# Optimization experiments

Measured on AMD Instinct MI355X. Metric: run time of the kernel, lower is better.

## Reference

```python
import jax, jax.numpy as jnp
import numpy as np

N = 50000   # nodes
E = 800000  # edges
F = 64      # input features
H = 64      # hidden (nhid)
C = 10      # classes
G = 500     # graphs in batch


def setup_inputs() -> dict:
    key = jax.random.key(0)
    ks = jax.random.split(key, 12)
    s = lambda fan: np.float32(1.0 / np.sqrt(fan))
    return {
        "x": jax.random.normal(ks[0], (N, F), jnp.float32),
        "edge_index": jax.random.randint(ks[1], (2, E), 0, N, dtype=jnp.int64),
        "batch": jnp.sort(jax.random.randint(ks[2], (N,), 0, G, dtype=jnp.int64)),
        "W1": jax.random.normal(ks[3], (F, H), jnp.float32) * s(F),
        "b1": jnp.zeros((H,), jnp.float32),
        "W2": jax.random.normal(ks[4], (H, H), jnp.float32) * s(H),
        "b2": jnp.zeros((H,), jnp.float32),
        "W3": jax.random.normal(ks[5], (H, H), jnp.float32) * s(H),
        "b3": jnp.zeros((H,), jnp.float32),
        "lin1_W": jax.random.normal(ks[6], (H, H), jnp.float32) * s(H),
        "lin1_b": jnp.zeros((H,), jnp.float32),
        "lin2_W": jax.random.normal(ks[7], (H, C), jnp.float32) * s(H),
        "lin2_b": jnp.zeros((C,), jnp.float32),
    }


def reference(x, edge_index, batch, W1, b1, W2, b2, W3, b3, lin1_W, lin1_b, lin2_W, lin2_b):
    n = x.shape[0]
    loops = jnp.arange(n, dtype=edge_index.dtype)
    src = jnp.concatenate([edge_index[0], loops])  # message sources (x_j)
    dst = jnp.concatenate([edge_index[1], loops])  # aggregation targets
    # symmetric GCN normalization on A + I
    deg = jax.ops.segment_sum(jnp.ones(src.shape, x.dtype), dst, num_segments=n)
    dis = jax.lax.rsqrt(deg)  # deg >= 1 thanks to self-loops
    norm = (dis[src] * dis[dst])[:, None]  # [E+N, 1]

    def gcn_relu(h, W, b):
        h = h @ W                                   # [N, H]
        agg = jax.ops.segment_sum(h[src] * norm, dst, num_segments=n)
        return jax.nn.relu(agg + b)

    h = gcn_relu(x, W1, b1)
    h = gcn_relu(h, W2, b2)
    h = gcn_relu(h, W3, b3)

    # global mean pool per graph
    sums = jax.ops.segment_sum(h, batch, num_segments=G)
    counts = jax.ops.segment_sum(jnp.ones((n,), h.dtype), batch, num_segments=G)
    pooled = sums / jnp.maximum(counts, 1.0)[:, None]  # [G, H]

    h = jax.nn.relu(pooled @ lin1_W + lin1_b)
    # dropout is identity in eval mode
    logits = h @ lin2_W + lin2_b
    return jax.nn.log_softmax(logits, axis=-1)
```

## Files before the change

### kernel.cpp

```cpp
#include <hip/hip_runtime.h>

#define NN 50000
#define NE 800000
#define HD 64
#define NC 10
#define NG 500
#define CAP 64
#define NBLK 196
#define NPART 8
#define PSZ 6250
#define FILLB 2048
#define NPW 8

__device__ __forceinline__ float bf16_to_f32(unsigned short h) {
    union { unsigned int u; float f; } v;
    v.u = ((unsigned int)h) << 16;
    return v.f;
}
__device__ __forceinline__ unsigned short f32_to_bf16(float f) {
    union { float f; unsigned int u; } v;
    v.f = f;
    unsigned int r = v.u + 0x7FFFu + ((v.u >> 16) & 1u);
    return (unsigned short)(r >> 16);
}

__global__ void init_k(int* __restrict__ rowcnt) {
    int i = blockIdx.x * 256 + threadIdx.x;
    if (i < NN) rowcnt[i] = 0;
}

__global__ __launch_bounds__(256) void fill3_k(
    const int* __restrict__ src, const int* __restrict__ dst,
    int* __restrict__ rowcnt, unsigned short* __restrict__ col16) {
    int part = blockIdx.x & (NPART - 1);
    int blk = blockIdx.x >> 3;
    int dlo = part * PSZ, dhi = dlo + PSZ;
    int stride = (FILLB / NPART) * 256;
    for (int e = blk * 256 + threadIdx.x; e < NE; e += stride) {
        int d = dst[e];
        if (d >= dlo && d < dhi) {
            int p = atomicAdd(&rowcnt[d], 1);
            if (p < CAP) col16[(size_t)d * CAP + p] = (unsigned short)src[e];
        }
    }
}

__global__ __launch_bounds__(256) void gemm64_k(const float* __restrict__ in,
                                                const float* __restrict__ W,
                                                const int* __restrict__ rowcnt,
                                                unsigned short* __restrict__ out16) {
    __shared__ float Ws[64 * 64];
    int t = threadIdx.x;
    for (int k = t; k < 64 * 64; k += 256) Ws[k] = W[k];
    __syncthreads();
    int lane = t & 63;
    int rgrp = t >> 6;
    int row0 = blockIdx.x * 16 + rgrp * 4;
#pragma unroll
    for (int rr = 0; rr < 4; ++rr) {
        int row = row0 + rr;
        const float4* h4 = (const float4*)(in + (size_t)row * HD);
        float acc = 0.f;
#pragma unroll
        for (int k4 = 0; k4 < 16; ++k4) {
            float4 h = h4[k4];
            acc += h.x * Ws[(k4 * 4 + 0) * 64 + lane];
            acc += h.y * Ws[(k4 * 4 + 1) * 64 + lane];
            acc += h.z * Ws[(k4 * 4 + 2) * 64 + lane];
            acc += h.w * Ws[(k4 * 4 + 3) * 64 + lane];
        }
        float di = rsqrtf((float)(rowcnt[row] + 1));
        out16[(size_t)row * HD + lane] = f32_to_bf16(acc * di);
    }
}

__global__ __launch_bounds__(256) void aggemm_k(
    const unsigned short* __restrict__ tin, const int* __restrict__ rowcnt,
    const unsigned short* __restrict__ col16, const float* __restrict__ bias,
    const float* __restrict__ Wn, unsigned short* __restrict__ tout) {
    __shared__ float Ws[64 * 64];
    __shared__ float rbuf[4][64];
    int t = threadIdx.x;
    for (int k = t; k < 64 * 64; k += 256) Ws[k] = Wn[k];
    __syncthreads();
    int w = t >> 6, lane = t & 63;
    float bv = bias[lane];
    int base = (blockIdx.x * 4 + w) * NPW;
    for (int n = 0; n < NPW; ++n) {
        int wid = base + n;
        bool valid = wid < NN;
        float r = 0.f, di = 1.f;
        if (valid) {
            int colv = col16[(size_t)wid * CAP + lane];
            int c0 = rowcnt[wid];
            di = rsqrtf((float)(c0 + 1));
            int cnt = c0 > CAP ? CAP : c0;
            float acc[8];
#pragma unroll
            for (int j = 0; j < 8; ++j) acc[j] = 0.f;
            acc[0] = bf16_to_f32(tin[(size_t)wid * HD + lane]);
            int e = 0;
            for (; e + 7 < cnt; e += 8) {
#pragma unroll
                for (int j = 0; j < 8; ++j) {
                    int s = __shfl(colv, e + j);
                    acc[j] += bf16_to_f32(tin[(size_t)s * HD + lane]);
                }
            }
            for (; e < cnt; ++e) {
                int s = __shfl(colv, e);
                acc[0] += bf16_to_f32(tin[(size_t)s * HD + lane]);
            }
            float s01 = (acc[0] + acc[1]) + (acc[2] + acc[3]);
            float s23 = (acc[4] + acc[5]) + (acc[6] + acc[7]);
            r = fmaxf((s01 + s23) * di + bv, 0.f);
        }
        rbuf[w][lane] = r;
        __builtin_amdgcn_wave_barrier();
        float acc2 = 0.f;
        const float4* rb4 = (const float4*)rbuf[w];
#pragma unroll
        for (int k4 = 0; k4 < 16; ++k4) {
            float4 rv = rb4[k4];
            acc2 += rv.x * Ws[(k4 * 4 + 0) * 64 + lane];
            acc2 += rv.y * Ws[(k4 * 4 + 1) * 64 + lane];
            acc2 += rv.z * Ws[(k4 * 4 + 2) * 64 + lane];
            acc2 += rv.w * Ws[(k4 * 4 + 3) * 64 + lane];
        }
        if (valid) tout[(size_t)wid * HD + lane] = f32_to_bf16(acc2 * di);
        __builtin_amdgcn_wave_barrier();
    }
}

__global__ __launch_bounds__(256) void agg_k(
    const unsigned short* __restrict__ tin, const int* __restrict__ rowcnt,
    const unsigned short* __restrict__ col16, const float* __restrict__ bias,
    float* __restrict__ out) {
    int wid = blockIdx.x * 4 + (threadIdx.x >> 6);
    int lane = threadIdx.x & 63;
    if (wid >= NN) return;
    int colv = col16[(size_t)wid * CAP + lane];
    int c0 = rowcnt[wid];
    float di = rsqrtf((float)(c0 + 1));
    int cnt = c0 > CAP ? CAP : c0;
    float acc[8];
#pragma unroll
    for (int j = 0; j < 8; ++j) acc[j] = 0.f;
    acc[0] = bf16_to_f32(tin[(size_t)wid * HD + lane]);
    int e = 0;
    for (; e + 7 < cnt; e += 8) {
#pragma unroll
        for (int j = 0; j < 8; ++j) {
            int s = __shfl(colv, e + j);
            acc[j] += bf16_to_f32(tin[(size_t)s * HD + lane]);
        }
    }
    for (; e < cnt; ++e) {
        int s = __shfl(colv, e);
        acc[0] += bf16_to_f32(tin[(size_t)s * HD + lane]);
    }
    float s01 = (acc[0] + acc[1]) + (acc[2] + acc[3]);
    float s23 = (acc[4] + acc[5]) + (acc[6] + acc[7]);
    out[(size_t)wid * HD + lane] = fmaxf((s01 + s23) * di + bias[lane], 0.f);
}

__global__ __launch_bounds__(256) void poolhead_k(
    const float* __restrict__ h, const int* __restrict__ batch,
    const float* __restrict__ l1W, const float* __restrict__ l1b,
    const float* __restrict__ l2W, const float* __restrict__ l2b,
    float* __restrict__ out) {
    __shared__ float part[4][64];
    __shared__ float p[64];
    __shared__ float hsm[64];
    __shared__ float lg[NC];
    __shared__ int ss[2];
    int g = blockIdx.x;
    int t = threadIdx.x, lane = t & 63, w = t >> 6;
    if (t < 2) {
        int target = g + t;
        int lo = 0, hi = NN;
        while (lo < hi) {
            int mid = (lo + hi) >> 1;
            if (batch[mid] < target) lo = mid + 1; else hi = mid;
        }
        ss[t] = lo;
    }
    __syncthreads();
    int s0 = ss[0], s1 = ss[1];
    float acc = 0.f;
    for (int i = s0 + w; i < s1; i += 4) acc += h[(size_t)i * HD + lane];
    part[w][lane] = acc;
    __syncthreads();
    if (t < 64) {
        float s = part[0][t] + part[1][t] + part[2][t] + part[3][t];
        float c = (float)(s1 - s0);
        p[t] = s / fmaxf(c, 1.0f);
    }
    __syncthreads();
    if (t < 64) {
        float a = l1b[t];
#pragma unroll
        for (int k = 0; k < 64; ++k) a += p[k] * l1W[k * 64 + t];
        hsm[t] = fmaxf(a, 0.f);
    }
    __syncthreads();
    if (t < NC) {
        float a = l2b[t];
#pragma unroll
        for (int k = 0; k < 64; ++k) a += hsm[k] * l2W[k * NC + t];
        lg[t] = a;
    }
    __syncthreads();
    if (t < NC) {
        float m = -1e30f;
#pragma unroll
        for (int k = 0; k < NC; ++k) m = fmaxf(m, lg[k]);
        float s = 0.f;
#pragma unroll
        for (int k = 0; k < NC; ++k) s += expf(lg[k] - m);
        out[(size_t)g * NC + t] = lg[t] - m - logf(s);
    }
}

extern "C" void kernel_launch(void* const* d_in, const int* in_sizes, int n_in,
                              void* d_out, int out_size, void* d_ws, size_t ws_size,
                              hipStream_t stream) {
    const float* x = (const float*)d_in[0];
    const int* ei = (const int*)d_in[1];
    const int* src = ei;
    const int* dst = ei + NE;
    const int* batch = (const int*)d_in[2];
    const float* W1 = (const float*)d_in[3];
    const float* b1 = (const float*)d_in[4];
    const float* W2 = (const float*)d_in[5];
    const float* b2 = (const float*)d_in[6];
    const float* W3 = (const float*)d_in[7];
    const float* b3 = (const float*)d_in[8];
    const float* l1W = (const float*)d_in[9];
    const float* l1b = (const float*)d_in[10];
    const float* l2W = (const float*)d_in[11];
    const float* l2b = (const float*)d_in[12];
    float* out = (float*)d_out;

    char* p = (char*)d_ws;
    auto alloc = [&](size_t bytes) {
        char* r = p;
        p += (bytes + 255) & ~(size_t)255;
        return r;
    };
    int* rowcnt = (int*)alloc(NN * 4);
    unsigned short* col16 = (unsigned short*)alloc((size_t)NN * CAP * 2);
    unsigned short* tmpA = (unsigned short*)alloc((size_t)NN * HD * 2);
    unsigned short* tmpB = (unsigned short*)alloc((size_t)NN * HD * 2);
    float* hcur = (float*)alloc((size_t)NN * HD * 4);

    const int AGB = (NN + 4 * NPW - 1) / (4 * NPW);

    init_k<<<NBLK, 256, 0, stream>>>(rowcnt);
    fill3_k<<<FILLB, 256, 0, stream>>>(src, dst, rowcnt, col16);

    gemm64_k<<<3125, 256, 0, stream>>>(x, W1, rowcnt, tmpA);
    aggemm_k<<<AGB, 256, 0, stream>>>(tmpA, rowcnt, col16, b1, W2, tmpB);
    aggemm_k<<<AGB, 256, 0, stream>>>(tmpB, rowcnt, col16, b2, W3, tmpA);
    agg_k<<<(NN + 3) / 4, 256, 0, stream>>>(tmpA, rowcnt, col16, b3, hcur);

    poolhead_k<<<NG, 256, 0, stream>>>(hcur, batch, l1W, l1b, l2W, l2b, out);
}
```

Baseline: 279.0 us.

## Use bf16 MFMA with split-weight precision for the 64x64 GCN transforms

Replaces the scalar FMA dense transforms (first-layer GEMM and the fused aggregate-then-GEMM kernels) with 16x16x32 bf16 MFMA instructions. The weights are split into high and low bf16 parts so the result stays close to fp32 on the weight side, while activations are rounded to bf16. The fused kernel now aggregates 64 rows per block into shared memory and then runs one block-wide MFMA tile, replacing per-row LDS dot products. This adds extra MFMA work for the split weights, keeps the weights in registers per wave, and lowers activation precision for the first layer's input.

```diff
diff --git a/kernel.cpp b/kernel.cpp
--- a/kernel.cpp
+++ b/kernel.cpp
@@ -10,7 +10,10 @@
 #define NPART 8
 #define PSZ 6250
 #define FILLB 2048
-#define NPW 8
+#define MBLK 782
+
+typedef float f32x4 __attribute__((ext_vector_type(4)));
+typedef short bf16x8 __attribute__((ext_vector_type(8)));
 
 __device__ __forceinline__ float bf16_to_f32(unsigned short h) {
     union { unsigned int u; float f; } v;
@@ -22,6 +25,23 @@
     v.f = f;
     unsigned int r = v.u + 0x7FFFu + ((v.u >> 16) & 1u);
     return (unsigned short)(r >> 16);
+}
+
+__device__ __forceinline__ void load_wfrags(const float* __restrict__ W, int lane,
+                                            bf16x8 bh[4][2], bf16x8 bl[4][2]) {
+    int col = lane & 15, krow = (lane >> 4) * 8;
+#pragma unroll
+    for (int n = 0; n < 4; ++n)
+#pragma unroll
+        for (int kt = 0; kt < 2; ++kt)
+#pragma unroll
+            for (int j = 0; j < 8; ++j) {
+                float wv = W[(kt * 32 + krow + j) * 64 + n * 16 + col];
+                unsigned short h = f32_to_bf16(wv);
+                float rem = wv - bf16_to_f32(h);
+                bh[n][kt][j] = (short)h;
+                bl[n][kt][j] = (short)f32_to_bf16(rem);
+            }
 }
 
 __global__ void init_k(int* __restrict__ rowcnt) {
@@ -45,52 +65,68 @@
     }
 }
 
-__global__ __launch_bounds__(256) void gemm64_k(const float* __restrict__ in,
-                                                const float* __restrict__ W,
-                                                const int* __restrict__ rowcnt,
-                                                unsigned short* __restrict__ out16) {
-    __shared__ float Ws[64 * 64];
-    int t = threadIdx.x;
-    for (int k = t; k < 64 * 64; k += 256) Ws[k] = W[k];
-    __syncthreads();
-    int lane = t & 63;
-    int rgrp = t >> 6;
-    int row0 = blockIdx.x * 16 + rgrp * 4;
-#pragma unroll
-    for (int rr = 0; rr < 4; ++rr) {
-        int row = row0 + rr;
-        const float4* h4 = (const float4*)(in + (size_t)row * HD);
-        float acc = 0.f;
-#pragma unroll
-        for (int k4 = 0; k4 < 16; ++k4) {
-            float4 h = h4[k4];
-            acc += h.x * Ws[(k4 * 4 + 0) * 64 + lane];
-            acc += h.y * Ws[(k4 * 4 + 1) * 64 + lane];
-            acc += h.z * Ws[(k4 * 4 + 2) * 64 + lane];
-            acc += h.w * Ws[(k4 * 4 + 3) * 64 + lane];
-        }
-        float di = rsqrtf((float)(rowcnt[row] + 1));
-        out16[(size_t)row * HD + lane] = f32_to_bf16(acc * di);
-    }
-}
-
-__global__ __launch_bounds__(256) void aggemm_k(
+__global__ __launch_bounds__(256) void mfma_gemm1_k(
+    const float* __restrict__ x, const float* __restrict__ W,
+    const int* __restrict__ rowcnt, unsigned short* __restrict__ out16) {
+    __shared__ unsigned short A[64][72];
+    int t = threadIdx.x, lane = t & 63, w = t >> 6;
+    int base = blockIdx.x * 64;
+#pragma unroll
+    for (int i = 0; i < 4; ++i) {
+        int idx = t + i * 256;
+        int row = idx >> 4, c4 = (idx & 15) * 4;
+        int r = base + row;
+        float4 v = make_float4(0.f, 0.f, 0.f, 0.f);
+        if (r < NN) v = ((const float4*)x)[(size_t)r * 16 + (idx & 15)];
+        unsigned int p0 = f32_to_bf16(v.x) | ((unsigned int)f32_to_bf16(v.y) << 16);
+        unsigned int p1 = f32_to_bf16(v.z) | ((unsigned int)f32_to_bf16(v.w) << 16);
+        *(unsigned int*)&A[row][c4] = p0;
+        *(unsigned int*)&A[row][c4 + 2] = p1;
+    }
+    bf16x8 bh[4][2], bl[4][2];
+    load_wfrags(W, lane, bh, bl);
+    __syncthreads();
+    int col = lane & 15, krow = (lane >> 4) * 8;
+    bf16x8 a0 = *(const bf16x8*)&A[w * 16 + col][krow];
+    bf16x8 a1 = *(const bf16x8*)&A[w * 16 + col][32 + krow];
+    f32x4 acc[4];
+#pragma unroll
+    for (int n = 0; n < 4; ++n) { acc[n] = (f32x4){0.f, 0.f, 0.f, 0.f}; }
+#pragma unroll
+    for (int n = 0; n < 4; ++n) {
+        acc[n] = __builtin_amdgcn_mfma_f32_16x16x32_bf16(a0, bh[n][0], acc[n], 0, 0, 0);
+        acc[n] = __builtin_amdgcn_mfma_f32_16x16x32_bf16(a1, bh[n][1], acc[n], 0, 0, 0);
+        acc[n] = __builtin_amdgcn_mfma_f32_16x16x32_bf16(a0, bl[n][0], acc[n], 0, 0, 0);
+        acc[n] = __builtin_amdgcn_mfma_f32_16x16x32_bf16(a1, bl[n][1], acc[n], 0, 0, 0);
+    }
+    int row0 = base + w * 16 + (lane >> 4) * 4;
+    float di[4];
+#pragma unroll
+    for (int r = 0; r < 4; ++r)
+        di[r] = (row0 + r < NN) ? rsqrtf((float)(rowcnt[row0 + r] + 1)) : 1.f;
+#pragma unroll
+    for (int n = 0; n < 4; ++n)
+#pragma unroll
+        for (int r = 0; r < 4; ++r) {
+            int row = row0 + r;
+            if (row < NN)
+                out16[(size_t)row * HD + n * 16 + col] = f32_to_bf16(acc[n][r] * di[r]);
+        }
+}
+
+__global__ __launch_bounds__(256) void agg_mfma_k(
     const unsigned short* __restrict__ tin, const int* __restrict__ rowcnt,
     const unsigned short* __restrict__ col16, const float* __restrict__ bias,
-    const float* __restrict__ Wn, unsigned short* __restrict__ tout) {
-    __shared__ float Ws[64 * 64];
-    __shared__ float rbuf[4][64];
-    int t = threadIdx.x;
-    for (int k = t; k < 64 * 64; k += 256) Ws[k] = Wn[k];
-    __syncthreads();
-    int w = t >> 6, lane = t & 63;
+    const float* __restrict__ W, unsigned short* __restrict__ tout) {
+    __shared__ unsigned short A[64][72];
+    __shared__ float dibuf[64];
+    int t = threadIdx.x, lane = t & 63, w = t >> 6;
+    int base = blockIdx.x * 64;
     float bv = bias[lane];
-    int base = (blockIdx.x * 4 + w) * NPW;
-    for (int n = 0; n < NPW; ++n) {
-        int wid = base + n;
-        bool valid = wid < NN;
+    for (int n16 = 0; n16 < 16; ++n16) {
+        int wid = base + w * 16 + n16;
         float r = 0.f, di = 1.f;
-        if (valid) {
+        if (wid < NN) {
             int colv = col16[(size_t)wid * CAP + lane];
             int c0 = rowcnt[wid];
             di = rsqrtf((float)(c0 + 1));
@@ -115,21 +151,37 @@
             float s23 = (acc[4] + acc[5]) + (acc[6] + acc[7]);
             r = fmaxf((s01 + s23) * di + bv, 0.f);
         }
-        rbuf[w][lane] = r;
-        __builtin_amdgcn_wave_barrier();
-        float acc2 = 0.f;
-        const float4* rb4 = (const float4*)rbuf[w];
-#pragma unroll
-        for (int k4 = 0; k4 < 16; ++k4) {
-            float4 rv = rb4[k4];
-            acc2 += rv.x * Ws[(k4 * 4 + 0) * 64 + lane];
-            acc2 += rv.y * Ws[(k4 * 4 + 1) * 64 + lane];
-            acc2 += rv.z * Ws[(k4 * 4 + 2) * 64 + lane];
-            acc2 += rv.w * Ws[(k4 * 4 + 3) * 64 + lane];
-        }
-        if (valid) tout[(size_t)wid * HD + lane] = f32_to_bf16(acc2 * di);
-        __builtin_amdgcn_wave_barrier();
-    }
+        A[w * 16 + n16][lane] = f32_to_bf16(r);
+        if (lane == 0) dibuf[w * 16 + n16] = di;
+    }
+    bf16x8 bh[4][2], bl[4][2];
+    load_wfrags(W, lane, bh, bl);
+    __syncthreads();
+    int col = lane & 15, krow = (lane >> 4) * 8;
+    bf16x8 a0 = *(const bf16x8*)&A[w * 16 + col][krow];
+    bf16x8 a1 = *(const bf16x8*)&A[w * 16 + col][32 + krow];
+    f32x4 acc[4];
+#pragma unroll
+    for (int n = 0; n < 4; ++n) { acc[n] = (f32x4){0.f, 0.f, 0.f, 0.f}; }
+#pragma unroll
+    for (int n = 0; n < 4; ++n) {
+        acc[n] = __builtin_amdgcn_mfma_f32_16x16x32_bf16(a0, bh[n][0], acc[n], 0, 0, 0);
+        acc[n] = __builtin_amdgcn_mfma_f32_16x16x32_bf16(a1, bh[n][1], acc[n], 0, 0, 0);
+        acc[n] = __builtin_amdgcn_mfma_f32_16x16x32_bf16(a0, bl[n][0], acc[n], 0, 0, 0);
+        acc[n] = __builtin_amdgcn_mfma_f32_16x16x32_bf16(a1, bl[n][1], acc[n], 0, 0, 0);
+    }
+    int row0 = base + w * 16 + (lane >> 4) * 4;
+    float dr[4];
+#pragma unroll
+    for (int r = 0; r < 4; ++r) dr[r] = dibuf[w * 16 + (lane >> 4) * 4 + r];
+#pragma unroll
+    for (int n = 0; n < 4; ++n)
+#pragma unroll
+        for (int r = 0; r < 4; ++r) {
+            int row = row0 + r;
+            if (row < NN)
+                tout[(size_t)row * HD + n * 16 + col] = f32_to_bf16(acc[n][r] * dr[r]);
+        }
 }
 
 __global__ __launch_bounds__(256) void agg_k(
@@ -254,14 +306,12 @@
     unsigned short* tmpB = (unsigned short*)alloc((size_t)NN * HD * 2);
     float* hcur = (float*)alloc((size_t)NN * HD * 4);
 
-    const int AGB = (NN + 4 * NPW - 1) / (4 * NPW);
-
     init_k<<<NBLK, 256, 0, stream>>>(rowcnt);
     fill3_k<<<FILLB, 256, 0, stream>>>(src, dst, rowcnt, col16);
 
-    gemm64_k<<<3125, 256, 0, stream>>>(x, W1, rowcnt, tmpA);
-    aggemm_k<<<AGB, 256, 0, stream>>>(tmpA, rowcnt, col16, b1, W2, tmpB);
-    aggemm_k<<<AGB, 256, 0, stream>>>(tmpB, rowcnt, col16, b2, W3, tmpA);
+    mfma_gemm1_k<<<MBLK, 256, 0, stream>>>(x, W1, rowcnt, tmpA);
+    agg_mfma_k<<<MBLK, 256, 0, stream>>>(tmpA, rowcnt, col16, b1, W2, tmpB);
+    agg_mfma_k<<<MBLK, 256, 0, stream>>>(tmpB, rowcnt, col16, b2, W3, tmpA);
     agg_k<<<(NN + 3) / 4, 256, 0, stream>>>(tmpA, rowcnt, col16, b3, hcur);
 
     poolhead_k<<<NG, 256, 0, stream>>>(hcur, batch, l1W, l1b, l2W, l2b, out);
```

Result: faster. 272.3 us (-2.4%).
